# Kernel tuning notes

Hardware: AMD Instinct MI355X
Metric: run time of the kernel (lower is better)

The kernel has to match this reference:

```python
import jax, jax.numpy as jnp
import numpy as np

N_NODES = 100000
N_EDGES = 1600000
IN_FEATS = 128
HIDDEN = 128
NUM_CLASSES = 64


def setup_inputs() -> dict:
    key = jax.random.key(0)
    k1, k2, k3, k4, k5 = jax.random.split(key, 5)
    inputs = jax.random.normal(k1, (N_NODES, IN_FEATS), dtype=jnp.float32)
    src = jax.random.randint(k2, (N_EDGES,), 0, N_NODES, dtype=jnp.int32)
    dst = jax.random.randint(k3, (N_EDGES,), 0, N_NODES, dtype=jnp.int32)
    W1 = jax.random.normal(k4, (IN_FEATS, HIDDEN), dtype=jnp.float32) / np.sqrt(IN_FEATS)
    b1 = jnp.zeros((HIDDEN,), dtype=jnp.float32)
    W2 = jax.random.normal(k5, (HIDDEN, NUM_CLASSES), dtype=jnp.float32) / np.sqrt(HIDDEN)
    b2 = jnp.zeros((NUM_CLASSES,), dtype=jnp.float32)
    return {"inputs": inputs, "src": src, "dst": dst, "W1": W1, "b1": b1, "W2": W2, "b2": b2}


def _graph_conv(x, src, dst, W, b, n_nodes):
    # DGL GraphConv, norm='both': h = D_in^{-1/2} A D_out^{-1/2} x W + b
    ones = jnp.ones(src.shape[0], dtype=x.dtype)
    deg_out = jax.ops.segment_sum(ones, src, num_segments=n_nodes)
    deg_in = jax.ops.segment_sum(ones, dst, num_segments=n_nodes)
    norm_src = jax.lax.rsqrt(jnp.clip(deg_out, 1.0))  # [N]
    norm_dst = jax.lax.rsqrt(jnp.clip(deg_in, 1.0))   # [N]
    x = x * norm_src[:, None]
    msgs = x[src]                                      # [E, d] gather
    agg = jax.ops.segment_sum(msgs, dst, num_segments=n_nodes)  # [N, d] scatter-add
    agg = agg * norm_dst[:, None]
    return agg @ W + b


def reference(inputs, src, dst, W1, b1, W2, b2):
    n = inputs.shape[0]
    h = _graph_conv(inputs, src, dst, W1, b1, n)
    h = jax.nn.relu(h)
    h = _graph_conv(h, src, dst, W2, b2, n)
    return h
```

## Files before the change

kernel.cpp:

```cpp
#include <hip/hip_runtime.h>
#include <hip/hip_bf16.h>

#define N_FEATS_IN 128
#define BK_BITS 8
#define BK_SIZE 256
#define EPB 4096
#define MAXNB 512

typedef _Float16 h8 __attribute__((ext_vector_type(8)));
typedef float    f4v __attribute__((ext_vector_type(4)));
typedef float    f8v __attribute__((ext_vector_type(8)));

__device__ inline int wave_incl_scan(int v) {
    const int lane = threadIdx.x & 63;
    for (int off = 1; off < 64; off <<= 1) {
        int u = __shfl_up(v, off, 64);
        if (lane >= off) v += u;
    }
    return v;
}

__device__ inline int block_excl_scan(int s, int* ws, int* total) {
    const int lane = threadIdx.x & 63, wid = threadIdx.x >> 6;
    int inc = wave_incl_scan(s);
    if (lane == 63) ws[wid] = inc;
    __syncthreads();
    int woff = 0;
#pragma unroll
    for (int w = 0; w < 4; ++w) woff += (w < wid) ? ws[w] : 0;
    if (total) *total = ws[0] + ws[1] + ws[2] + ws[3];
    return woff + inc - s;
}

__global__ __launch_bounds__(256) void hist_kernel(
    const int* __restrict__ src, const int* __restrict__ dst,
    int* __restrict__ bh_d, int* __restrict__ bh_s, int E, int NB) {
    __shared__ int hd[MAXNB];
    __shared__ int hs[MAXNB];
    const int t = threadIdx.x;
    for (int i = t; i < NB; i += 256) { hd[i] = 0; hs[i] = 0; }
    __syncthreads();
    const int base = blockIdx.x * EPB;
    const int end = min(base + EPB, E);
    for (int e = base + t; e < end; e += 256) {
        atomicAdd(&hd[dst[e] >> BK_BITS], 1);
        atomicAdd(&hs[src[e] >> BK_BITS], 1);
    }
    __syncthreads();
    for (int i = t; i < NB; i += 256) {
        bh_d[(size_t)blockIdx.x * NB + i] = hd[i];
        bh_s[(size_t)blockIdx.x * NB + i] = hs[i];
    }
}

__global__ __launch_bounds__(256) void colprefix2_kernel(
    int* __restrict__ bh_d, int* __restrict__ bh_s,
    int* __restrict__ tot_d, int* __restrict__ tot_s, int NBLK, int NB) {
    __shared__ int ws[4];
    const int b = blockIdx.x;
    const int t = threadIdx.x;
    int carry = 0;
    for (int base = 0; base < NBLK; base += 256) {
        const int r = base + t;
        const int v = (r < NBLK) ? bh_d[(size_t)r * NB + b] : 0;
        int total;
        const int e = block_excl_scan(v, ws, &total);
        if (r < NBLK) bh_d[(size_t)r * NB + b] = carry + e;
        carry += total;
        __syncthreads();
    }
    if (t == 0) tot_d[b] = carry;
    carry = 0;
    for (int base = 0; base < NBLK; base += 256) {
        const int r = base + t;
        const int v = (r < NBLK) ? bh_s[(size_t)r * NB + b] : 0;
        int total;
        const int e = block_excl_scan(v, ws, &total);
        if (r < NBLK) bh_s[(size_t)r * NB + b] = carry + e;
        carry += total;
        __syncthreads();
    }
    if (t == 0) tot_s[b] = carry;
}

__global__ __launch_bounds__(256) void bscan2_kernel(
    const int* __restrict__ tot_d, const int* __restrict__ tot_s,
    int* __restrict__ gb_d, int* __restrict__ gb_s,
    int* __restrict__ row_ptr, int NB, int N, int E) {
    __shared__ int ws[4];
    const int t = threadIdx.x;
    {
        const int a = (2 * t < NB) ? tot_d[2 * t] : 0;
        const int b = (2 * t + 1 < NB) ? tot_d[2 * t + 1] : 0;
        const int excl = block_excl_scan(a + b, ws, nullptr);
        if (2 * t < NB) gb_d[2 * t] = excl;
        if (2 * t + 1 < NB) gb_d[2 * t + 1] = excl + a;
    }
    __syncthreads();
    {
        const int a = (2 * t < NB) ? tot_s[2 * t] : 0;
        const int b = (2 * t + 1 < NB) ? tot_s[2 * t + 1] : 0;
        const int excl = block_excl_scan(a + b, ws, nullptr);
        if (2 * t < NB) gb_s[2 * t] = excl;
        if (2 * t + 1 < NB) gb_s[2 * t + 1] = excl + a;
    }
    if (t == 0) { gb_d[NB] = E; gb_s[NB] = E; row_ptr[N] = E; }
}

__global__ __launch_bounds__(256) void scatter2_kernel(
    const int* __restrict__ src, const int* __restrict__ dst,
    const int* __restrict__ bh_d, const int* __restrict__ bh_s,
    const int* __restrict__ gb_d, const int* __restrict__ gb_s,
    unsigned int* __restrict__ ebuf, unsigned char* __restrict__ sbuf,
    int E, int NB) {
    __shared__ int cd[MAXNB];
    __shared__ int cs[MAXNB];
    const int t = threadIdx.x;
    for (int i = t; i < NB; i += 256) {
        cd[i] = bh_d[(size_t)blockIdx.x * NB + i] + gb_d[i];
        cs[i] = bh_s[(size_t)blockIdx.x * NB + i] + gb_s[i];
    }
    __syncthreads();
    const int base = blockIdx.x * EPB;
    const int end = min(base + EPB, E);
    for (int e = base + t; e < end; e += 256) {
        const int d = dst[e];
        const int s = src[e];
        const int pd = atomicAdd(&cd[d >> BK_BITS], 1);
        ebuf[pd] = ((unsigned)s << 8) | (unsigned)(d & (BK_SIZE - 1));
        const int ps = atomicAdd(&cs[s >> BK_BITS], 1);
        sbuf[ps] = (unsigned char)(s & (BK_SIZE - 1));
    }
}

__global__ __launch_bounds__(256) void bucket_csr_kernel(
    const unsigned int* __restrict__ ebuf, const int* __restrict__ gb_d,
    const unsigned char* __restrict__ sbuf, const int* __restrict__ gb_s,
    int* __restrict__ row_ptr, float* __restrict__ norm_dst,
    float* __restrict__ norm_src, int* __restrict__ edge_src, int N) {
    __shared__ int cnt[BK_SIZE];
    __shared__ int lro[BK_SIZE];
    __shared__ int ws[4];
    const int b = blockIdx.x;
    const int t = threadIdx.x;
    const int beg = gb_d[b], end = gb_d[b + 1];
    const int node = b * BK_SIZE + t;

    cnt[t] = 0;
    __syncthreads();
    for (int j = beg + t; j < end; j += 256)
        atomicAdd(&cnt[ebuf[j] & (BK_SIZE - 1)], 1);
    __syncthreads();

    const int v = cnt[t];
    const int excl = block_excl_scan(v, ws, nullptr);
    lro[t] = beg + excl;
    if (node < N) {
        row_ptr[node] = beg + excl;
        norm_dst[node] = rsqrtf(fmaxf((float)v, 1.0f));
    }
    __syncthreads();
    cnt[t] = 0;
    __syncthreads();

    for (int j = beg + t; j < end; j += 256) {
        const unsigned int ed = ebuf[j];
        const int dl = ed & (BK_SIZE - 1);
        const int p = atomicAdd(&cnt[dl], 1);
        edge_src[lro[dl] + p] = (int)(ed >> 8);
    }

    __syncthreads();
    cnt[t] = 0;
    __syncthreads();
    const int sb = gb_s[b], se = gb_s[b + 1];
    for (int j = sb + t; j < se; j += 256)
        atomicAdd(&cnt[sbuf[j]], 1);
    __syncthreads();
    if (node < N)
        norm_src[node] = rsqrtf(fmaxf((float)cnt[t], 1.0f));
}

template <int OC, bool XHALF>
__global__ __launch_bounds__(256) void mfma_gemm_kernel(
    const void* __restrict__ Xv, const float* __restrict__ W,
    const float* __restrict__ scale, _Float16* __restrict__ Y, int n) {
    constexpr int K = 128;
    constexpr int NT = OC / 16;
    constexpr int RPB = 128;
    __shared__ _Float16 Wf[NT * 4 * 64 * 8];

    const int tid = threadIdx.x;
    for (int i = tid; i < K * OC; i += 256) {
        const int k = i / OC, c = i % OC;
        const int t = c >> 4, s = k >> 5, q = (k >> 3) & 3, j = k & 7;
        Wf[(((t * 4 + s) * 4 + q) * 16 + (c & 15)) * 8 + j] = (_Float16)W[i];
    }
    __syncthreads();

    const int lane = tid & 63;
    const int wv = tid >> 6;
    const int m = lane & 15, q = lane >> 4;

#pragma unroll
    for (int it = 0; it < RPB / 64; ++it) {
        const int rbase = blockIdx.x * RPB + it * 64 + wv * 16;
        const int lrow = min(rbase + m, n - 1);

        h8 a[4];
        if constexpr (XHALF) {
            const _Float16* X = (const _Float16*)Xv;
            const _Float16* p = &X[(size_t)lrow * K + q * 8];
#pragma unroll
            for (int s = 0; s < 4; ++s) a[s] = *(const h8*)(p + s * 32);
        } else {
            const float* X = (const float*)Xv;
            const float* p = &X[(size_t)lrow * K + q * 8];
#pragma unroll
            for (int s = 0; s < 4; ++s) {
                const float4 u0 = *(const float4*)(p + s * 32);
                const float4 u1 = *(const float4*)(p + s * 32 + 4);
                h8 v;
                v[0] = (_Float16)u0.x; v[1] = (_Float16)u0.y;
                v[2] = (_Float16)u0.z; v[3] = (_Float16)u0.w;
                v[4] = (_Float16)u1.x; v[5] = (_Float16)u1.y;
                v[6] = (_Float16)u1.z; v[7] = (_Float16)u1.w;
                a[s] = v;
            }
        }

        f4v acc[NT];
#pragma unroll
        for (int t = 0; t < NT; ++t) acc[t] = (f4v)0.0f;

#pragma unroll
        for (int s = 0; s < 4; ++s) {
#pragma unroll
            for (int t = 0; t < NT; ++t) {
                const h8 b = *(const h8*)&Wf[((t * 4 + s) * 64 + lane) * 8];
                acc[t] = __builtin_amdgcn_mfma_f32_16x16x32_f16(
                    a[s], b, acc[t], 0, 0, 0);
            }
        }

#pragma unroll
        for (int r = 0; r < 4; ++r) {
            const int orow = rbase + q * 4 + r;
            if (orow < n) {
                const float sc = scale[orow];
#pragma unroll
                for (int t = 0; t < NT; ++t)
                    Y[(size_t)orow * OC + t * 16 + m] =
                        (_Float16)(acc[t][r] * sc);
            }
        }
    }
}

template <int FEAT, bool RELU, bool OUT_HALF>
__global__ __launch_bounds__(256) void gather_agg_kernel(
    const _Float16* __restrict__ T, const int* __restrict__ row_ptr,
    const int* __restrict__ edge_src, const float* __restrict__ norm_dst,
    const float* __restrict__ bias, void* __restrict__ outv, int n) {
    constexpr int TPN = FEAT / 8;
    constexpr int NPB = 256 / TPN;
    const int node = blockIdx.x * NPB + threadIdx.x / TPN;
    const int f8 = threadIdx.x % TPN;
    if (node >= n) return;
    const int beg = row_ptr[node];
    const int end = row_ptr[node + 1];
    const h8* T8 = (const h8*)T;

    f8v acc = (f8v)0.0f;
    int j = beg;
    for (; j + 7 < end; j += 8) {
        int s[8];
#pragma unroll
        for (int u = 0; u < 8; ++u) s[u] = edge_src[j + u];
        h8 a[8];
#pragma unroll
        for (int u = 0; u < 8; ++u) a[u] = T8[(size_t)s[u] * TPN + f8];
#pragma unroll
        for (int u = 0; u < 8; ++u)
            acc += __builtin_convertvector(a[u], f8v);
    }
    for (; j + 3 < end; j += 4) {
        int s[4];
#pragma unroll
        for (int u = 0; u < 4; ++u) s[u] = edge_src[j + u];
        h8 a[4];
#pragma unroll
        for (int u = 0; u < 4; ++u) a[u] = T8[(size_t)s[u] * TPN + f8];
#pragma unroll
        for (int u = 0; u < 4; ++u)
            acc += __builtin_convertvector(a[u], f8v);
    }
    for (; j < end; ++j)
        acc += __builtin_convertvector(T8[(size_t)edge_src[j] * TPN + f8], f8v);

    const float nd = norm_dst[node];
    float r[8];
#pragma unroll
    for (int k = 0; k < 8; ++k) {
        r[k] = acc[k] * nd + bias[f8 * 8 + k];
        if constexpr (RELU) r[k] = fmaxf(r[k], 0.0f);
    }

    if constexpr (OUT_HALF) {
        _Float16* out = (_Float16*)outv;
        h8 o;
#pragma unroll
        for (int k = 0; k < 8; ++k) o[k] = (_Float16)r[k];
        *(h8*)&out[(size_t)node * FEAT + f8 * 8] = o;
    } else {
        float* out = (float*)outv;
        float4 o0 = make_float4(r[0], r[1], r[2], r[3]);
        float4 o1 = make_float4(r[4], r[5], r[6], r[7]);
        *(float4*)&out[(size_t)node * FEAT + f8 * 8] = o0;
        *(float4*)&out[(size_t)node * FEAT + f8 * 8 + 4] = o1;
    }
}

extern "C" void kernel_launch(void* const* d_in, const int* in_sizes, int n_in,
                              void* d_out, int out_size, void* d_ws, size_t ws_size,
                              hipStream_t stream) {
    const float* x   = (const float*)d_in[0];
    const int*   src = (const int*)d_in[1];
    const int*   dst = (const int*)d_in[2];
    const float* W1  = (const float*)d_in[3];
    const float* b1  = (const float*)d_in[4];
    const float* W2  = (const float*)d_in[5];
    const float* b2  = (const float*)d_in[6];
    float* out = (float*)d_out;

    const int N = in_sizes[0] / N_FEATS_IN;
    const int E = in_sizes[1];
    const int NB = (N + BK_SIZE - 1) / BK_SIZE;
    const int NBLK = (E + EPB - 1) / EPB;

    auto align4 = [](size_t w) { return (w + 3) & ~(size_t)3; };
    char* base = (char*)d_ws;
    size_t off = 0;
    auto take = [&](size_t words) {
        char* p = base + off * 4;
        off = align4(off + words);
        return p;
    };
    int*   tot_d    = (int*)take(NB);
    int*   tot_s    = (int*)take(NB);
    int*   gb_d     = (int*)take(NB + 1);
    int*   gb_s     = (int*)take(NB + 1);
    int*   bh_d     = (int*)take((size_t)NBLK * NB);
    int*   bh_s     = (int*)take((size_t)NBLK * NB);
    unsigned int*  ebuf = (unsigned int*)take(E);
    unsigned char* sbuf = (unsigned char*)take((E + 3) / 4);
    int*   row_ptr  = (int*)take(N + 1);
    int*   edge_src = (int*)take(E);
    float* norms    = (float*)take(2 * (size_t)N);
    _Float16* t1    = (_Float16*)take((size_t)N * 64);
    _Float16* h1    = (_Float16*)take((size_t)N * 64);
    _Float16* t2    = (_Float16*)take((size_t)N * 32);
    float* norm_src = norms;
    float* norm_dst = norms + N;

    hist_kernel<<<NBLK, 256, 0, stream>>>(src, dst, bh_d, bh_s, E, NB);
    colprefix2_kernel<<<NB, 256, 0, stream>>>(bh_d, bh_s, tot_d, tot_s,
                                              NBLK, NB);
    bscan2_kernel<<<1, 256, 0, stream>>>(tot_d, tot_s, gb_d, gb_s, row_ptr,
                                         NB, N, E);
    scatter2_kernel<<<NBLK, 256, 0, stream>>>(src, dst, bh_d, bh_s, gb_d, gb_s,
                                              ebuf, sbuf, E, NB);
    bucket_csr_kernel<<<NB, 256, 0, stream>>>(ebuf, gb_d, sbuf, gb_s, row_ptr,
                                              norm_dst, norm_src, edge_src, N);

    mfma_gemm_kernel<128, false><<<(N + 127) / 128, 256, 0, stream>>>(
        x, W1, norm_src, t1, N);
    gather_agg_kernel<128, true, true><<<(N + 15) / 16, 256, 0, stream>>>(
        t1, row_ptr, edge_src, norm_dst, b1, h1, N);

    mfma_gemm_kernel<64, true><<<(N + 127) / 128, 256, 0, stream>>>(
        h1, W2, norm_src, t2, N);
    gather_agg_kernel<64, false, false><<<(N + 31) / 32, 256, 0, stream>>>(
        t2, row_ptr, edge_src, norm_dst, b2, out, N);
}
```

Before: 335.1 us.

## Fuse layer-1 aggregation with layer-2 GEMM into one MFMA kernel

Replaces the layer-1 gather/aggregate kernel and the second GEMM with a single kernel. Each block aggregates 16 nodes, applies bias, ReLU and the source norm, stages the fp16 rows in shared memory, and multiplies them by W2 with MFMA. This removes the h1 intermediate round-trip to global memory and one kernel launch. In exchange, every block converts and reswizzles all of W2 into shared memory, which adds redundant per-block work across many small blocks.

```diff
diff --git a/kernel.cpp b/kernel.cpp
--- a/kernel.cpp
+++ b/kernel.cpp
@@ -318,6 +318,101 @@
         float4 o1 = make_float4(r[4], r[5], r[6], r[7]);
         *(float4*)&out[(size_t)node * FEAT + f8 * 8] = o0;
         *(float4*)&out[(size_t)node * FEAT + f8 * 8 + 4] = o1;
+    }
+}
+
+template <int FEAT, int OC>
+__global__ __launch_bounds__(256) void gather_gemm_kernel(
+    const _Float16* __restrict__ T, const int* __restrict__ row_ptr,
+    const int* __restrict__ edge_src, const float* __restrict__ norm_dst,
+    const float* __restrict__ norm_src, const float* __restrict__ bias,
+    const float* __restrict__ W, _Float16* __restrict__ Y, int n) {
+    constexpr int TPN = FEAT / 8;
+    constexpr int NPB = 256 / TPN;
+    constexpr int NT = OC / 16;
+    constexpr int AP = FEAT + 8;
+    __shared__ _Float16 Wf[NT * 4 * 64 * 8];
+    __shared__ _Float16 Ah[NPB * AP];
+
+    const int tid = threadIdx.x;
+    for (int i = tid; i < FEAT * OC; i += 256) {
+        const int k = i / OC, c = i % OC;
+        const int t = c >> 4, s = k >> 5, q = (k >> 3) & 3, j = k & 7;
+        Wf[(((t * 4 + s) * 4 + q) * 16 + (c & 15)) * 8 + j] = (_Float16)W[i];
+    }
+
+    const int node = blockIdx.x * NPB + tid / TPN;
+    const int f8 = tid % TPN;
+    const int nl = tid / TPN;
+    const h8* T8 = (const h8*)T;
+
+    float r[8];
+    if (node < n) {
+        const int beg = row_ptr[node];
+        const int end = row_ptr[node + 1];
+        f8v acc = (f8v)0.0f;
+        int j = beg;
+        for (; j + 7 < end; j += 8) {
+            int s[8];
+#pragma unroll
+            for (int u = 0; u < 8; ++u) s[u] = edge_src[j + u];
+            h8 a[8];
+#pragma unroll
+            for (int u = 0; u < 8; ++u) a[u] = T8[(size_t)s[u] * TPN + f8];
+#pragma unroll
+            for (int u = 0; u < 8; ++u)
+                acc += __builtin_convertvector(a[u], f8v);
+        }
+        for (; j + 3 < end; j += 4) {
+            int s[4];
+#pragma unroll
+            for (int u = 0; u < 4; ++u) s[u] = edge_src[j + u];
+            h8 a[4];
+#pragma unroll
+            for (int u = 0; u < 4; ++u) a[u] = T8[(size_t)s[u] * TPN + f8];
+#pragma unroll
+            for (int u = 0; u < 4; ++u)
+                acc += __builtin_convertvector(a[u], f8v);
+        }
+        for (; j < end; ++j)
+            acc += __builtin_convertvector(T8[(size_t)edge_src[j] * TPN + f8],
+                                           f8v);
+
+        const float nd = norm_dst[node];
+        const float ns = norm_src[node];
+#pragma unroll
+        for (int k = 0; k < 8; ++k) {
+            float v = acc[k] * nd + bias[f8 * 8 + k];
+            v = fmaxf(v, 0.0f);
+            r[k] = v * ns;
+        }
+    } else {
+#pragma unroll
+        for (int k = 0; k < 8; ++k) r[k] = 0.0f;
+    }
+
+    {
+        h8 av;
+#pragma unroll
+        for (int k = 0; k < 8; ++k) av[k] = (_Float16)r[k];
+        *(h8*)&Ah[nl * AP + f8 * 8] = av;
+    }
+    __syncthreads();
+
+    const int lane = tid & 63, w = tid >> 6;
+    const int m = lane & 15, q = lane >> 4;
+    f4v acc2 = (f4v)0.0f;
+#pragma unroll
+    for (int s = 0; s < 4; ++s) {
+        const h8 a = *(const h8*)&Ah[m * AP + s * 32 + q * 8];
+        const h8 b = *(const h8*)&Wf[((w * 4 + s) * 64 + lane) * 8];
+        acc2 = __builtin_amdgcn_mfma_f32_16x16x32_f16(a, b, acc2, 0, 0, 0);
+    }
+#pragma unroll
+    for (int rr = 0; rr < 4; ++rr) {
+        const int orow = blockIdx.x * NPB + q * 4 + rr;
+        if (orow < n)
+            Y[(size_t)orow * OC + w * 16 + m] = (_Float16)acc2[rr];
     }
 }
 
@@ -358,7 +453,6 @@
     int*   edge_src = (int*)take(E);
     float* norms    = (float*)take(2 * (size_t)N);
     _Float16* t1    = (_Float16*)take((size_t)N * 64);
-    _Float16* h1    = (_Float16*)take((size_t)N * 64);
     _Float16* t2    = (_Float16*)take((size_t)N * 32);
     float* norm_src = norms;
     float* norm_dst = norms + N;
@@ -375,11 +469,10 @@
 
     mfma_gemm_kernel<128, false><<<(N + 127) / 128, 256, 0, stream>>>(
         x, W1, norm_src, t1, N);
-    gather_agg_kernel<128, true, true><<<(N + 15) / 16, 256, 0, stream>>>(
-        t1, row_ptr, edge_src, norm_dst, b1, h1, N);
-
-    mfma_gemm_kernel<64, true><<<(N + 127) / 128, 256, 0, stream>>>(
-        h1, W2, norm_src, t2, N);
+
+    gather_gemm_kernel<128, 64><<<(N + 15) / 16, 256, 0, stream>>>(
+        t1, row_ptr, edge_src, norm_dst, norm_src, b1, W2, t2, N);
+
     gather_agg_kernel<64, false, false><<<(N + 31) / 32, 256, 0, stream>>>(
         t2, row_ptr, edge_src, norm_dst, b2, out, N);
 }
```

Result: faster. 325.2 us (-3.0%).
